# Kernel optimization log

Measured on AMD Instinct MI355X. Metric: run time of the kernel, lower is better.

## Reference

```python
import jax, jax.numpy as jnp
import numpy as np


def setup_inputs() -> dict:
    key = jax.random.key(0)
    k1, k2, k3 = jax.random.split(key, 3)
    N, T, C, H, W, D = 2, 8, 3, 128, 128, 64
    images = jax.random.normal(k1, (N, T, C, H, W), dtype=jnp.float32)
    # well-conditioned pinhole intrinsics: f ~ 100, principal point near center
    K = jnp.array([[100.0, 0.0, W / 2.0], [0.0, 100.0, H / 2.0], [0.0, 0.0, 1.0]], jnp.float32)
    intrinsics = K[None, None] + 0.1 * jax.random.normal(k2, (N, T, 3, 3), dtype=jnp.float32)
    # near-identity extrinsics with small perturbation; last row kept [0,0,0,1]
    E = jnp.eye(4, dtype=jnp.float32)[None, None] + 0.05 * jax.random.normal(k3, (N, T, 4, 4), dtype=jnp.float32)
    extrinsics = E.at[:, :, 3, :].set(jnp.array([0.0, 0.0, 0.0, 1.0], jnp.float32))
    depths = jnp.linspace(1.0, 64.0, D, dtype=jnp.float32)
    return {"images": images, "intrinsics": intrinsics, "extrinsics": extrinsics, "depths": depths}


def _homography_forward(images, intrinsics, extrinsics, depths):
    N, T, C, H, W = images.shape
    D = depths.shape[0]
    dt = images.dtype

    # --- get_homographies ---
    K_ref = intrinsics[:, 0]                      # (N,3,3)
    R_ref = extrinsics[:, 0, :3, :3]              # (N,3,3)
    t_ref = extrinsics[:, 0, :3, 3]               # (N,3)
    n_ref = extrinsics[:, 0, 2, :3]               # (N,3)
    R_view = extrinsics[:, :, :3, :3]             # (N,T,3,3)
    t_view = extrinsics[:, :, :3, 3]              # (N,T,3)

    a = jnp.einsum('nji,nj->ni', R_ref, t_ref)        # R_ref^T t_ref
    b = jnp.einsum('ntji,ntj->nti', R_view, t_view)   # R_view^T t_view
    diff = a[:, None, :] - b                          # (N,T,3)
    t_diff = diff[..., :, None] * n_ref[:, None, None, :]  # outer product -> (N,T,3,3)

    eye = jnp.eye(3, dtype=dt)
    Hmat = eye - t_diff[:, :, None] / depths[None, None, :, None, None]  # (N,T,D,3,3)

    KR = jnp.einsum('ntij,ntjk->ntik', intrinsics, R_view)          # K_view R_view
    world = jnp.einsum('ntij,ntdjk->ntdik', KR, Hmat)               # (N,T,D,3,3)
    ref = jnp.einsum('nij,njk->nik', R_ref, jnp.linalg.inv(K_ref))  # R_ref K_ref^-1
    homog = jnp.einsum('ntdij,njk->ntdik', world, ref)              # (N,T,D,3,3)

    # --- images_to_coords: cartesian_prod(x over W outer, y over H inner, z=1) ---
    x = jnp.arange(W, dtype=dt) + 0.5
    y = jnp.arange(H, dtype=dt) + 0.5
    xs, ys = jnp.meshgrid(x, y, indexing='ij')  # (W,H): x varies slowest
    coords = jnp.stack([xs.ravel(), ys.ravel(), jnp.ones(W * H, dt)], axis=-1)  # (WH,3)

    # --- warp ---
    nc = jnp.einsum('ntdij,pj->ntdpi', homog, coords)  # (N,T,D,WH,3)
    z = nc[..., 2]
    z = jnp.where(z == 0, jnp.asarray(1e-7, dt), z)
    grid = nc[..., :2] / z[..., None]                  # pixel-space coords (faithful: NOT normalized)
    grid = grid.reshape(N * T, D, H, W, 2)

    # --- grid_sample, bilinear, zeros padding, align_corners=False; all D planes at once ---
    gx = ((grid[..., 0] + 1.0) * W - 1.0) * 0.5        # (NT,D,H,W)
    gy = ((grid[..., 1] + 1.0) * H - 1.0) * 0.5
    x0 = jnp.floor(gx); x1 = x0 + 1.0
    y0 = jnp.floor(gy); y1 = y0 + 1.0
    wx1 = gx - x0; wx0 = 1.0 - wx1
    wy1 = gy - y0; wy0 = 1.0 - wy1

    flat = images.reshape(N * T, C, H * W)

    def corner(ix, iy, w):
        valid = (ix >= 0) & (ix <= W - 1) & (iy >= 0) & (iy <= H - 1)
        ii = (jnp.clip(iy, 0, H - 1) * W + jnp.clip(ix, 0, W - 1)).astype(jnp.int32)
        ii = ii.reshape(N * T, -1)                                   # (NT, D*H*W)
        px = jax.vmap(lambda im, idx: im[:, idx])(flat, ii)          # (NT, C, D*H*W)
        return px * (w * valid.astype(dt)).reshape(N * T, 1, -1)

    out = (corner(x0, y0, wx0 * wy0) + corner(x1, y0, wx1 * wy0)
           + corner(x0, y1, wx0 * wy1) + corner(x1, y1, wx1 * wy1))
    return out.reshape(N, T, C, D, H, W)


def reference(images, intrinsics, extrinsics, depths):
    return _homography_forward(images, intrinsics, extrinsics, depths)
```

## Files before the change

kernel.cpp:

```cpp
#include <hip/hip_runtime.h>
#include <hip/hip_bf16.h>

#define Nn 2
#define Tt 8
#define Cc 3
#define Hh 128
#define Ww 128
#define Dd 64
#define NT (Nn * Tt)
#define HW (Hh * Ww)

typedef float f32x4 __attribute__((ext_vector_type(4)));

__global__ __launch_bounds__(256) void homog_fused(
    const float* __restrict__ images,
    const float* __restrict__ intr,
    const float* __restrict__ extr,
    const float* __restrict__ depths,
    float* __restrict__ out)
{
    const int d  = blockIdx.y;
    const int nt = blockIdx.z;

    __shared__ float Ms[12];

    if (threadIdx.x == 0) {
        const int n = nt >> 3;
        const float* Kv = intr + nt * 9;
        const float* Kr = intr + (n * Tt) * 9;
        const float* Ev = extr + nt * 16;
        const float* Er = extr + (n * Tt) * 16;

        float Rr[3][3], Rv[3][3], tr[3], tv[3];
        #pragma unroll
        for (int i = 0; i < 3; ++i) {
            #pragma unroll
            for (int j = 0; j < 3; ++j) {
                Rr[i][j] = Er[i * 4 + j];
                Rv[i][j] = Ev[i * 4 + j];
            }
            tr[i] = Er[i * 4 + 3];
            tv[i] = Ev[i * 4 + 3];
        }

        float diff[3];
        #pragma unroll
        for (int i = 0; i < 3; ++i) {
            float a = Rr[0][i] * tr[0] + Rr[1][i] * tr[1] + Rr[2][i] * tr[2];
            float b = Rv[0][i] * tv[0] + Rv[1][i] * tv[1] + Rv[2][i] * tv[2];
            diff[i] = a - b;
        }
        float nr[3] = {Rr[2][0], Rr[2][1], Rr[2][2]};

        float k0 = Kr[0], k1 = Kr[1], k2 = Kr[2];
        float k3 = Kr[3], k4 = Kr[4], k5 = Kr[5];
        float k6 = Kr[6], k7 = Kr[7], k8 = Kr[8];
        float c00 = k4 * k8 - k5 * k7;
        float c01 = k5 * k6 - k3 * k8;
        float c02 = k3 * k7 - k4 * k6;
        float det = k0 * c00 + k1 * c01 + k2 * c02;
        float invd = 1.0f / det;
        float iK[3][3];
        iK[0][0] = c00 * invd;
        iK[0][1] = (k2 * k7 - k1 * k8) * invd;
        iK[0][2] = (k1 * k5 - k2 * k4) * invd;
        iK[1][0] = c01 * invd;
        iK[1][1] = (k0 * k8 - k2 * k6) * invd;
        iK[1][2] = (k2 * k3 - k0 * k5) * invd;
        iK[2][0] = c02 * invd;
        iK[2][1] = (k1 * k6 - k0 * k7) * invd;
        iK[2][2] = (k0 * k4 - k1 * k3) * invd;

        float refM[3][3], KR[3][3];
        #pragma unroll
        for (int i = 0; i < 3; ++i)
            #pragma unroll
            for (int j = 0; j < 3; ++j) {
                refM[i][j] = Rr[i][0] * iK[0][j] + Rr[i][1] * iK[1][j] + Rr[i][2] * iK[2][j];
                KR[i][j]   = Kv[i * 3 + 0] * Rv[0][j] + Kv[i * 3 + 1] * Rv[1][j] + Kv[i * 3 + 2] * Rv[2][j];
            }

        float W0[3][3], u[3], v[3];
        #pragma unroll
        for (int i = 0; i < 3; ++i) {
            #pragma unroll
            for (int j = 0; j < 3; ++j)
                W0[i][j] = KR[i][0] * refM[0][j] + KR[i][1] * refM[1][j] + KR[i][2] * refM[2][j];
            u[i] = KR[i][0] * diff[0] + KR[i][1] * diff[1] + KR[i][2] * diff[2];
            v[i] = refM[0][i] * nr[0] + refM[1][i] * nr[1] + refM[2][i] * nr[2];
        }

        const float rdep = __builtin_amdgcn_rcpf(depths[d]);
        #pragma unroll
        for (int i = 0; i < 3; ++i) {
            float ui = u[i] * rdep;
            #pragma unroll
            for (int j = 0; j < 3; ++j)
                Ms[i * 4 + j] = W0[i][j] - ui * v[j];
        }
    }
    __syncthreads();

    const f32x4 row0 = *reinterpret_cast<const f32x4*>(&Ms[0]);
    const f32x4 row1 = *reinterpret_cast<const f32x4*>(&Ms[4]);
    const f32x4 row2 = *reinterpret_cast<const f32x4*>(&Ms[8]);
    const float m0 = row0.x, m1 = row0.y, m2 = row0.z;
    const float m3 = row1.x, m4 = row1.y, m5 = row1.z;
    const float m6 = row2.x, m7 = row2.y, m8 = row2.z;

    const int q  = blockIdx.x * 256 + threadIdx.x;
    const int p0 = q << 2;
    const int h  = p0 >> 7;
    const int w  = p0 & 127;

    const float xc = (float)h + 0.5f;
    const float yc = (float)w + 0.5f;
    const float n0 = fmaf(m1, yc, fmaf(m0, xc, m2));
    const float n1 = fmaf(m4, yc, fmaf(m3, xc, m5));
    const float n2 = fmaf(m7, yc, fmaf(m6, xc, m8));

    float r0[4], r1[4], r2[4];
    #pragma unroll
    for (int k = 0; k < 4; ++k) { r0[k] = 0.0f; r1[k] = 0.0f; r2[k] = 0.0f; }

    {
        const float e0 = fmaf(3.0f, m1, n0);
        const float e1 = fmaf(3.0f, m4, n1);
        const float e2 = fmaf(3.0f, m7, n2);
        const float T  = fmaf(1.02f, fmaxf(fabsf(n2), fabsf(e2)), 1e-6f);
        const float mn0 = (n0 * e0 > 0.0f) ? fminf(fabsf(n0), fabsf(e0)) : 0.0f;
        const float mn1 = (n1 * e1 > 0.0f) ? fminf(fabsf(n1), fabsf(e1)) : 0.0f;
        const bool anyq = (mn0 <= T) && (mn1 <= T);

        if (anyq) {
            const float* img = images + nt * (Cc * HW);
            float a0 = n0, a1 = n1, a2 = n2;
            #pragma unroll
            for (int k = 0; k < 4; ++k) {
                float t = fmaf(1.02f, fabsf(a2), 1e-6f);
                if (fabsf(a0) <= t && fabsf(a1) <= t) {
                    float z  = (a2 == 0.0f) ? 1e-7f : a2;
                    float rz = __builtin_amdgcn_rcpf(z);
                    float gx = ((a0 * rz + 1.0f) * (float)Ww - 1.0f) * 0.5f;
                    float gy = ((a1 * rz + 1.0f) * (float)Hh - 1.0f) * 0.5f;

                    float x0f = floorf(gx), y0f = floorf(gy);
                    float x1f = x0f + 1.0f, y1f = y0f + 1.0f;
                    float wx1 = gx - x0f, wx0 = 1.0f - wx1;
                    float wy1 = gy - y0f, wy0 = 1.0f - wy1;

                    float v00 = (x0f >= 0.0f && x0f <= 127.0f && y0f >= 0.0f && y0f <= 127.0f) ? 1.0f : 0.0f;
                    float v10 = (x1f >= 0.0f && x1f <= 127.0f && y0f >= 0.0f && y0f <= 127.0f) ? 1.0f : 0.0f;
                    float v01 = (x0f >= 0.0f && x0f <= 127.0f && y1f >= 0.0f && y1f <= 127.0f) ? 1.0f : 0.0f;
                    float v11 = (x1f >= 0.0f && x1f <= 127.0f && y1f >= 0.0f && y1f <= 127.0f) ? 1.0f : 0.0f;

                    float w00 = (wx0 * wy0) * v00;
                    float w10 = (wx1 * wy0) * v10;
                    float w01 = (wx0 * wy1) * v01;
                    float w11 = (wx1 * wy1) * v11;

                    if (w00 != 0.0f || w10 != 0.0f || w01 != 0.0f || w11 != 0.0f) {
                        int xi0 = (int)fminf(fmaxf(x0f, 0.0f), 127.0f);
                        int xi1 = (int)fminf(fmaxf(x1f, 0.0f), 127.0f);
                        int yi0 = (int)fminf(fmaxf(y0f, 0.0f), 127.0f);
                        int yi1 = (int)fminf(fmaxf(y1f, 0.0f), 127.0f);
                        int i00 = yi0 * Ww + xi0;
                        int i10 = yi0 * Ww + xi1;
                        int i01 = yi1 * Ww + xi0;
                        int i11 = yi1 * Ww + xi1;
                        r0[k] = img[i00] * w00 + img[i10] * w10 + img[i01] * w01 + img[i11] * w11;
                        r1[k] = img[HW + i00] * w00 + img[HW + i10] * w10 + img[HW + i01] * w01 + img[HW + i11] * w11;
                        r2[k] = img[2 * HW + i00] * w00 + img[2 * HW + i10] * w10 + img[2 * HW + i01] * w01 + img[2 * HW + i11] * w11;
                    }
                }
                a0 += m1; a1 += m4; a2 += m7;
            }
        }
    }

    size_t obase = ((size_t)(nt * Cc) * Dd + d) * HW + p0;
    f32x4 s0 = {r0[0], r0[1], r0[2], r0[3]};
    f32x4 s1 = {r1[0], r1[1], r1[2], r1[3]};
    f32x4 s2 = {r2[0], r2[1], r2[2], r2[3]};
    __builtin_nontemporal_store(s0, reinterpret_cast<f32x4*>(&out[obase]));
    __builtin_nontemporal_store(s1, reinterpret_cast<f32x4*>(&out[obase + (size_t)Dd * HW]));
    __builtin_nontemporal_store(s2, reinterpret_cast<f32x4*>(&out[obase + (size_t)2 * Dd * HW]));
}

extern "C" void kernel_launch(void* const* d_in, const int* in_sizes, int n_in,
                              void* d_out, int out_size, void* d_ws, size_t ws_size,
                              hipStream_t stream) {
    const float* images = (const float*)d_in[0];
    const float* intr   = (const float*)d_in[1];
    const float* extr   = (const float*)d_in[2];
    const float* depths = (const float*)d_in[3];
    float* out = (float*)d_out;

    homog_fused<<<dim3(HW / 1024, Dd, NT), dim3(256), 0, stream>>>(
        images, intr, extr, depths, out);
}
```

Measured before the change: 36.67 us.

## Split channels across blocks and use regular stores instead of nontemporal

The grid is expanded threefold so each block handles a single color channel. Each thread now computes one channel's bilinear samples and writes one float4 instead of three. This adds parallelism and cuts per-thread register and memory pressure, at the cost of tripling the per-block homography setup and the coordinate/weight computation. It also replaces the nontemporal stores with ordinary cached stores, which changes how the large output write interacts with the cache.

```diff
diff --git a/kernel.cpp b/kernel.cpp
--- a/kernel.cpp
+++ b/kernel.cpp
@@ -19,8 +19,10 @@
     const float* __restrict__ depths,
     float* __restrict__ out)
 {
-    const int d  = blockIdx.y;
-    const int nt = blockIdx.z;
+    const int d     = blockIdx.y;
+    const int nt    = blockIdx.z;
+    const int c     = blockIdx.x >> 4;
+    const int chunk = blockIdx.x & 15;
 
     __shared__ float Ms[12];
 
@@ -108,8 +110,7 @@
     const float m3 = row1.x, m4 = row1.y, m5 = row1.z;
     const float m6 = row2.x, m7 = row2.y, m8 = row2.z;
 
-    const int q  = blockIdx.x * 256 + threadIdx.x;
-    const int p0 = q << 2;
+    const int p0 = (chunk * 256 + threadIdx.x) << 2;
     const int h  = p0 >> 7;
     const int w  = p0 & 127;
 
@@ -119,9 +120,7 @@
     const float n1 = fmaf(m4, yc, fmaf(m3, xc, m5));
     const float n2 = fmaf(m7, yc, fmaf(m6, xc, m8));
 
-    float r0[4], r1[4], r2[4];
-    #pragma unroll
-    for (int k = 0; k < 4; ++k) { r0[k] = 0.0f; r1[k] = 0.0f; r2[k] = 0.0f; }
+    float r[4] = {0.0f, 0.0f, 0.0f, 0.0f};
 
     {
         const float e0 = fmaf(3.0f, m1, n0);
@@ -130,10 +129,9 @@
         const float T  = fmaf(1.02f, fmaxf(fabsf(n2), fabsf(e2)), 1e-6f);
         const float mn0 = (n0 * e0 > 0.0f) ? fminf(fabsf(n0), fabsf(e0)) : 0.0f;
         const float mn1 = (n1 * e1 > 0.0f) ? fminf(fabsf(n1), fabsf(e1)) : 0.0f;
-        const bool anyq = (mn0 <= T) && (mn1 <= T);
 
-        if (anyq) {
-            const float* img = images + nt * (Cc * HW);
+        if (mn0 <= T && mn1 <= T) {
+            const float* img = images + (nt * Cc + c) * HW;
             float a0 = n0, a1 = n1, a2 = n2;
             #pragma unroll
             for (int k = 0; k < 4; ++k) {
@@ -168,9 +166,7 @@
                         int i10 = yi0 * Ww + xi1;
                         int i01 = yi1 * Ww + xi0;
                         int i11 = yi1 * Ww + xi1;
-                        r0[k] = img[i00] * w00 + img[i10] * w10 + img[i01] * w01 + img[i11] * w11;
-                        r1[k] = img[HW + i00] * w00 + img[HW + i10] * w10 + img[HW + i01] * w01 + img[HW + i11] * w11;
-                        r2[k] = img[2 * HW + i00] * w00 + img[2 * HW + i10] * w10 + img[2 * HW + i01] * w01 + img[2 * HW + i11] * w11;
+                        r[k] = img[i00] * w00 + img[i10] * w10 + img[i01] * w01 + img[i11] * w11;
                     }
                 }
                 a0 += m1; a1 += m4; a2 += m7;
@@ -178,13 +174,9 @@
         }
     }
 
-    size_t obase = ((size_t)(nt * Cc) * Dd + d) * HW + p0;
-    f32x4 s0 = {r0[0], r0[1], r0[2], r0[3]};
-    f32x4 s1 = {r1[0], r1[1], r1[2], r1[3]};
-    f32x4 s2 = {r2[0], r2[1], r2[2], r2[3]};
-    __builtin_nontemporal_store(s0, reinterpret_cast<f32x4*>(&out[obase]));
-    __builtin_nontemporal_store(s1, reinterpret_cast<f32x4*>(&out[obase + (size_t)Dd * HW]));
-    __builtin_nontemporal_store(s2, reinterpret_cast<f32x4*>(&out[obase + (size_t)2 * Dd * HW]));
+    const size_t ob = ((size_t)(nt * Cc + c) * Dd + d) * HW + p0;
+    f32x4 s = {r[0], r[1], r[2], r[3]};
+    *reinterpret_cast<f32x4*>(&out[ob]) = s;
 }
 
 extern "C" void kernel_launch(void* const* d_in, const int* in_sizes, int n_in,
@@ -196,6 +188,6 @@
     const float* depths = (const float*)d_in[3];
     float* out = (float*)d_out;
 
-    homog_fused<<<dim3(HW / 1024, Dd, NT), dim3(256), 0, stream>>>(
+    homog_fused<<<dim3(48, Dd, NT), dim3(256), 0, stream>>>(
         images, intr, extr, depths, out);
 }
```

Result: slower. 41.53 us (+13.3%).
